# Optimization experiments

Hardware: AMD Instinct MI355X
Metric: run time of the kernel (lower is better)

The kernel has to match this reference:

```python
import jax, jax.numpy as jnp
import numpy as np

N_NODES = 100000
N_EDGES = 3200000
NUM_TYPES = 8
TYPE_DIM = 16
IN_DIM = 5
HID = 64
HEADS = 2
OUT = 64
LN_EPS = 1e-5
NEG_SLOPE = 0.2


def segment_softmax(logits, seg, num_segments):
    # logits: [E, H], seg: [E] destination ids
    m = jax.ops.segment_max(logits, seg, num_segments=num_segments)
    m = jnp.where(jnp.isfinite(m), m, 0.0)
    e = jnp.exp(logits - m[seg])
    s = jax.ops.segment_sum(e, seg, num_segments=num_segments)
    return e / (s[seg] + 1e-16)


def gat_conv(x, W, a_src, a_dst, b, src, dst, n_nodes, heads, ch):
    # x: [N, F_in], W: [F_in, heads*ch], a_src/a_dst: [heads, ch], b: [heads*ch]
    h = (x @ W).reshape(n_nodes, heads, ch)            # [N, H, C]
    al_s = jnp.einsum('nhc,hc->nh', h, a_src)          # [N, H]
    al_d = jnp.einsum('nhc,hc->nh', h, a_dst)          # [N, H]
    e = jax.nn.leaky_relu(al_s[src] + al_d[dst], NEG_SLOPE)  # [E, H]
    alpha = segment_softmax(e, dst, n_nodes)           # [E, H]
    msg = alpha[:, :, None] * h[src]                   # [E, H, C]
    out = jax.ops.segment_sum(msg, dst, num_segments=n_nodes)  # [N, H, C]
    return out.reshape(n_nodes, heads * ch) + b


def setup_inputs() -> dict:
    key = jax.random.key(0)
    ks = jax.random.split(key, 16)
    in1 = IN_DIM + TYPE_DIM  # 21
    inp = {
        'x': jax.random.normal(ks[0], (N_NODES, IN_DIM), dtype=jnp.float32),
        'edge_index': jax.random.randint(ks[1], (2, N_EDGES), 0, N_NODES, dtype=jnp.int32),
        'type_ids': jax.random.randint(ks[2], (N_NODES,), 0, NUM_TYPES, dtype=jnp.int32),
        'type_emb': jax.random.normal(ks[3], (NUM_TYPES, TYPE_DIM), dtype=jnp.float32) * 0.3,
        'W1': jax.random.normal(ks[4], (in1, HID), dtype=jnp.float32) * (1.0 / np.sqrt(in1)),
        'a_src1': jax.random.normal(ks[5], (HEADS, HID // HEADS), dtype=jnp.float32) * 0.1,
        'a_dst1': jax.random.normal(ks[6], (HEADS, HID // HEADS), dtype=jnp.float32) * 0.1,
        'b1': jnp.zeros((HID,), dtype=jnp.float32),
        'W2': jax.random.normal(ks[7], (HID, OUT), dtype=jnp.float32) * (1.0 / np.sqrt(HID)),
        'a_src2': jax.random.normal(ks[8], (1, OUT), dtype=jnp.float32) * 0.1,
        'a_dst2': jax.random.normal(ks[9], (1, OUT), dtype=jnp.float32) * 0.1,
        'b2': jnp.zeros((OUT,), dtype=jnp.float32),
        'gamma': jnp.ones((OUT,), dtype=jnp.float32),
        'beta': jnp.zeros((OUT,), dtype=jnp.float32),
    }
    return inp


def reference(x, type_emb, W1, a_src1, a_dst1, b1, W2, a_src2, a_dst2, b2, gamma, beta, edge_index, type_ids):
    n = x.shape[0]
    # type embedding concat
    xin = jnp.concatenate([x, type_emb[type_ids]], axis=1)  # [N, 21]
    # add self loops (PyG GATConv default)
    loops = jnp.arange(n, dtype=edge_index.dtype)
    src = jnp.concatenate([edge_index[0], loops])
    dst = jnp.concatenate([edge_index[1], loops])
    h = gat_conv(xin, W1, a_src1, a_dst1, b1, src, dst, n, HEADS, HID // HEADS)
    h = jax.nn.relu(h)  # dropout = identity at inference
    h = gat_conv(h, W2, a_src2, a_dst2, b2, src, dst, n, 1, OUT)
    # LayerNorm
    mu = jnp.mean(h, axis=-1, keepdims=True)
    var = jnp.var(h, axis=-1, keepdims=True)
    return (h - mu) / jnp.sqrt(var + LN_EPS) * gamma + beta
```

## Files before the change

kernel.cpp:

```cpp
#include <hip/hip_runtime.h>
#include <hip/hip_fp16.h>

#define NEG_SLOPE 0.2f
#define INVLN2 1.44269504088896f
#define BKT_SHIFT 7
#define BKT_NODES 128
#define BKT_CAP 5120
#define SRC_SHIFT 18
#define SRC_MASK 0x3FFFF
#define CHUNK 4096
#define NBMAX 1024

typedef _Float16 half8 __attribute__((ext_vector_type(8)));
typedef float float4v __attribute__((ext_vector_type(4)));

__global__ void k_bucketA(const int* __restrict__ ei, unsigned int* __restrict__ pk,
                          int* __restrict__ bcnt, int E, int NBKT)
{
    __shared__ unsigned int stage[CHUNK];
    __shared__ unsigned short stageB[CHUNK];
    __shared__ int cnt[NBMAX];
    __shared__ int excl[NBMAX];
    __shared__ int curp[NBMAX];
    __shared__ int gbase[NBMAX];

    int t = threadIdx.x;
    int e0 = blockIdx.x * CHUNK;
    bool vec4 = ((E & 3) == 0);

    for (int i = t; i < NBMAX; i += 256) cnt[i] = 0;
    __syncthreads();

    int4 s4[4], d4[4];
    bool val[4];

    if (vec4) {
#pragma unroll
        for (int it = 0; it < 4; it++) {
            int e = e0 + it * 1024 + t * 4;
            val[it] = (e < E);
            if (val[it]) {
                s4[it] = *(const int4*)(ei + e);
                d4[it] = *(const int4*)(ei + (size_t)E + e);
                atomicAdd(&cnt[d4[it].x >> BKT_SHIFT], 1);
                atomicAdd(&cnt[d4[it].y >> BKT_SHIFT], 1);
                atomicAdd(&cnt[d4[it].z >> BKT_SHIFT], 1);
                atomicAdd(&cnt[d4[it].w >> BKT_SHIFT], 1);
            }
        }
    } else {
        for (int i = t; i < CHUNK; i += 256) {
            int e = e0 + i;
            if (e >= E) break;
            atomicAdd(&cnt[ei[E + e] >> BKT_SHIFT], 1);
        }
    }
    __syncthreads();
    for (int i = t; i < NBMAX; i += 256) curp[i] = cnt[i];
    __syncthreads();
    for (int off = 1; off < NBMAX; off <<= 1) {
        int v0 = (t       >= off) ? cnt[t       - off] : 0;
        int v1 = (t + 256 >= off) ? cnt[t + 256 - off] : 0;
        int v2 = (t + 512 >= off) ? cnt[t + 512 - off] : 0;
        int v3 = (t + 768 >= off) ? cnt[t + 768 - off] : 0;
        __syncthreads();
        cnt[t] += v0; cnt[t + 256] += v1; cnt[t + 512] += v2; cnt[t + 768] += v3;
        __syncthreads();
    }
    for (int i = t; i < NBMAX; i += 256) {
        int o = curp[i];
        int ex = cnt[i] - o;
        excl[i] = ex;
        curp[i] = ex;
    }
    __syncthreads();
    for (int b = t; b < NBKT; b += 256) {
        int c = cnt[b] - excl[b];
        gbase[b] = (c > 0) ? atomicAdd(&bcnt[b], c) : 0;
    }
    __syncthreads();
    if (vec4) {
#pragma unroll
        for (int it = 0; it < 4; it++) {
            if (!val[it]) continue;
            int ss[4] = {s4[it].x, s4[it].y, s4[it].z, s4[it].w};
            int dd[4] = {d4[it].x, d4[it].y, d4[it].z, d4[it].w};
#pragma unroll
            for (int k = 0; k < 4; k++) {
                int b = dd[k] >> BKT_SHIFT;
                int p = atomicAdd(&curp[b], 1);
                stage[p] = (unsigned)ss[k] | ((unsigned)(dd[k] & (BKT_NODES - 1)) << SRC_SHIFT);
                stageB[p] = (unsigned short)b;
            }
        }
    } else {
        for (int i = t; i < CHUNK; i += 256) {
            int e = e0 + i;
            if (e >= E) break;
            int s = ei[e], d = ei[E + e];
            int b = d >> BKT_SHIFT;
            int p = atomicAdd(&curp[b], 1);
            stage[p] = (unsigned)s | ((unsigned)(d & (BKT_NODES - 1)) << SRC_SHIFT);
            stageB[p] = (unsigned short)b;
        }
    }
    __syncthreads();
    int total = E - e0; if (total > CHUNK) total = CHUNK;
    for (int i = t; i < total; i += 256) {
        int b = stageB[i];
        int idx = gbase[b] + (i - excl[b]);
        if (idx < BKT_CAP) pk[(size_t)b * BKT_CAP + idx] = stage[i];
    }
}

__global__ __launch_bounds__(256) void k_build_node1(
        const unsigned int* __restrict__ pk, const int* __restrict__ bcnt,
        int* __restrict__ rs, int* __restrict__ cur, int* __restrict__ ssrc,
        const float* __restrict__ x, const int* __restrict__ type_ids,
        const float* __restrict__ type_emb, const float* __restrict__ W1,
        const float* __restrict__ a_src1, const float* __restrict__ a_dst1,
        __half2* __restrict__ h1h, float* __restrict__ als1, float* __restrict__ ald1,
        int N, int NBKT)
{
    __shared__ unsigned int vals[BKT_CAP];
    __shared__ int cnt[BKT_NODES];
    __shared__ int cursor[BKT_NODES];
    __shared__ int orig[BKT_NODES];
    __shared__ int red[256];
    int t = threadIdx.x;

    if (blockIdx.x >= NBKT) {
        int node = (blockIdx.x - NBKT) * 4 + (t >> 6);
        int j = t & 63;
        if (node >= N) return;

        float xin[21];
#pragma unroll
        for (int k = 0; k < 5; k++) xin[k] = x[node * 5 + k];
        int ty = type_ids[node];
#pragma unroll
        for (int k = 0; k < 16; k++) xin[5 + k] = type_emb[ty * 16 + k];

        float h = 0.f;
#pragma unroll
        for (int k = 0; k < 21; k++) h += xin[k] * W1[k * 64 + j];

        float hn = __shfl_xor(h, 1);
        if ((j & 1) == 0)
            h1h[node * 32 + (j >> 1)] = __floats2half2_rn(h, hn);

        int head = j >> 5, lane = j & 31;
        float ps = h * a_src1[head * 32 + lane];
        float pd = h * a_dst1[head * 32 + lane];
#pragma unroll
        for (int m = 16; m >= 1; m >>= 1) { ps += __shfl_xor(ps, m); pd += __shfl_xor(pd, m); }
        if (lane == 0) {
            als1[node * 2 + head] = ps * INVLN2;
            ald1[node * 2 + head] = pd * INVLN2;
        }
        return;
    }

    int b = blockIdx.x;
    int nb = min(bcnt[b], BKT_CAP);

    int part = 0;
    for (int i = t; i < b; i += 256) part += min(bcnt[i], BKT_CAP);
    red[t] = part;
    if (t < BKT_NODES) cnt[t] = 0;
    __syncthreads();
    for (int off = 128; off; off >>= 1) {
        if (t < off) red[t] += red[t + off];
        __syncthreads();
    }
    int bs = red[0];

    const unsigned int* mypk = pk + (size_t)b * BKT_CAP;
    int nb4 = nb & ~3;
    for (int e = t * 4; e < nb4; e += 1024) {
        uint4 v = *(const uint4*)(mypk + e);
        *(uint4*)(vals + e) = v;
        atomicAdd(&cnt[v.x >> SRC_SHIFT], 1);
        atomicAdd(&cnt[v.y >> SRC_SHIFT], 1);
        atomicAdd(&cnt[v.z >> SRC_SHIFT], 1);
        atomicAdd(&cnt[v.w >> SRC_SHIFT], 1);
    }
    for (int e = nb4 + t; e < nb; e += 256) {
        unsigned int v = mypk[e];
        vals[e] = v;
        atomicAdd(&cnt[v >> SRC_SHIFT], 1);
    }
    __syncthreads();
    if (t < BKT_NODES) orig[t] = cnt[t];
    __syncthreads();
    for (int off = 1; off < BKT_NODES; off <<= 1) {
        int v = 0;
        if (t < BKT_NODES && t >= off) v = cnt[t - off];
        __syncthreads();
        if (t < BKT_NODES) cnt[t] += v;
        __syncthreads();
    }
    if (t < BKT_NODES) {
        int c = orig[t];
        int ex = cnt[t] - c;
        cursor[t] = ex;
        int node = (b << BKT_SHIFT) + t;
        if (node < N) { rs[node] = bs + ex; cur[node] = bs + ex + c; }
    }
    __syncthreads();
    for (int e = t; e < nb; e += 256) {
        unsigned int w = vals[e];
        int p = atomicAdd(&cursor[w >> SRC_SHIFT], 1);
        ssrc[bs + p] = (int)(w & SRC_MASK);
    }
}

__global__ void k_gather1(const int* __restrict__ rs, const int* __restrict__ cur,
                          const int* __restrict__ ssrc, const float4* __restrict__ h4,
                          const float* __restrict__ als1, const float* __restrict__ ald1,
                          const float* __restrict__ b1, float4* __restrict__ h2h4, int N)
{
    int node = blockIdx.x * 4 + (threadIdx.x >> 6);
    if (node >= N) return;
    int l = threadIdx.x & 63;
    int eg = l >> 3;
    int ch = l & 7;
    int head = ch >> 2;
    float ad = ald1[node * 2 + head];

    int beg = rs[node], end = cur[node];
    int cnt = end - beg;
    __half2 acc2[4];
    acc2[0] = acc2[1] = acc2[2] = acc2[3] = __float2half2_rn(0.f);
    float wsum = 0.f;

    int s0c = (eg < cnt) ? ssrc[beg + eg] : node;
    int s1c = (8 + eg < cnt) ? ssrc[beg + 8 + eg] : node;
    float al0c = als1[s0c * 2 + head];
    float al1c = als1[s1c * 2 + head];
    float4 r0c = h4[(size_t)s0c * 8 + ch];
    float4 r1c = h4[(size_t)s1c * 8 + ch];

    for (int base = 0; base < cnt; base += 16) {
        int n0 = base + 16 + eg, n1 = base + 24 + eg;
        int s0n = (n0 < cnt) ? ssrc[beg + n0] : node;
        int s1n = (n1 < cnt) ? ssrc[beg + n1] : node;
        float al0n = als1[s0n * 2 + head];
        float al1n = als1[s1n * 2 + head];
        float4 r0n = h4[(size_t)s0n * 8 + ch];
        float4 r1n = h4[(size_t)s1n * 8 + ch];

        bool v0 = (base + eg) < cnt, v1 = (base + 8 + eg) < cnt;
        float lg0 = al0c + ad; lg0 = (lg0 >= 0.f) ? lg0 : NEG_SLOPE * lg0;
        float lg1 = al1c + ad; lg1 = (lg1 >= 0.f) ? lg1 : NEG_SLOPE * lg1;
        float w0 = v0 ? exp2f(lg0) : 0.f;
        float w1 = v1 ? exp2f(lg1) : 0.f;
        __half2 wh0 = __float2half2_rn(w0);
        __half2 wh1 = __float2half2_rn(w1);
        const __half2* p0 = (const __half2*)&r0c;
        const __half2* p1 = (const __half2*)&r1c;
#pragma unroll
        for (int q = 0; q < 4; q++) {
            acc2[q] = __hfma2(p0[q], wh0, acc2[q]);
            acc2[q] = __hfma2(p1[q], wh1, acc2[q]);
        }
        wsum += w0 + w1;

        s0c = s0n; s1c = s1n; al0c = al0n; al1c = al1n; r0c = r0n; r1c = r1n;
    }
    float acc[8];
#pragma unroll
    for (int q = 0; q < 4; q++) {
        float2 f = __half22float2(acc2[q]);
        acc[2*q] = f.x; acc[2*q+1] = f.y;
    }
#pragma unroll
    for (int m = 8; m <= 32; m <<= 1) {
        wsum += __shfl_xor(wsum, m);
#pragma unroll
        for (int q = 0; q < 8; q++) acc[q] += __shfl_xor(acc[q], m);
    }
    {
        float lg = als1[node * 2 + head] + ad;
        lg = (lg >= 0.f) ? lg : NEG_SLOPE * lg;
        float w = exp2f(lg);
        float4 r = h4[(size_t)node * 8 + ch];
        const __half2* p = (const __half2*)&r;
#pragma unroll
        for (int q = 0; q < 4; q++) {
            float2 f = __half22float2(p[q]);
            acc[2*q] += w * f.x; acc[2*q+1] += w * f.y;
        }
        wsum += w;
    }
    float inv = 1.f / (wsum + 1e-16f);
    if (eg == 0) {
        union { float4 f4; __half2 h2[4]; } u;
#pragma unroll
        for (int q = 0; q < 4; q++) {
            float v0 = fmaxf(acc[2*q]   * inv + b1[ch * 8 + 2*q],     0.f);
            float v1 = fmaxf(acc[2*q+1] * inv + b1[ch * 8 + 2*q + 1], 0.f);
            u.h2[q] = __floats2half2_rn(v0, v1);
        }
        h2h4[(size_t)node * 8 + ch] = u.f4;
    }
}

__global__ __launch_bounds__(256) void k_node2m(
        const _Float16* __restrict__ h2h, const float* __restrict__ W2,
        const float* __restrict__ a_src2, const float* __restrict__ a_dst2,
        _Float16* __restrict__ h3h, float* __restrict__ als2, float* __restrict__ ald2, int N)
{
    __shared__ _Float16 w2t[64][72];
    __shared__ float h3t[4][16][65];
    int t = threadIdx.x;
    for (int e = t; e < 4096; e += 256) {
        int k = e >> 6, n = e & 63;
        w2t[n][k] = (_Float16)W2[e];
    }
    __syncthreads();

    int w = t >> 6, l = t & 63;
    int l15 = l & 15, quad = l >> 4;
    int nodebase = blockIdx.x * 64 + w * 16;

    int arow = nodebase + l15;
    if (arow >= N) arow = N - 1;
    const half8* ap = (const half8*)(h2h + (size_t)arow * 64 + quad * 8);
    half8 a0 = ap[0];
    half8 a1 = ap[4];
    float4v accs[4];
#pragma unroll
    for (int nt = 0; nt < 4; nt++) {
        half8 b0 = *(const half8*)(&w2t[nt * 16 + l15][quad * 8]);
        half8 b1 = *(const half8*)(&w2t[nt * 16 + l15][32 + quad * 8]);
        float4v c = {0.f, 0.f, 0.f, 0.f};
        c = __builtin_amdgcn_mfma_f32_16x16x32_f16(a0, b0, c, 0, 0, 0);
        c = __builtin_amdgcn_mfma_f32_16x16x32_f16(a1, b1, c, 0, 0, 0);
        accs[nt] = c;
    }
#pragma unroll
    for (int nt = 0; nt < 4; nt++)
#pragma unroll
        for (int r = 0; r < 4; r++)
            h3t[w][quad * 4 + r][nt * 16 + l15] = accs[nt][r];
    __syncthreads();

    int m = l >> 2, part = l & 3;
    int g = blockIdx.x * 64 + w * 16 + m;
    float ps = 0.f, pd = 0.f;
    union { float4 f4[2]; _Float16 h[16]; } u;
#pragma unroll
    for (int c = 0; c < 16; c++) {
        float v = h3t[w][m][part * 16 + c];
        ps += v * a_src2[part * 16 + c];
        pd += v * a_dst2[part * 16 + c];
        u.h[c] = (_Float16)v;
    }
    if (g < N) {
        float4* dst = (float4*)(h3h + (size_t)g * 64) + part * 2;
        dst[0] = u.f4[0];
        dst[1] = u.f4[1];
    }
    ps += __shfl_xor(ps, 1); ps += __shfl_xor(ps, 2);
    pd += __shfl_xor(pd, 1); pd += __shfl_xor(pd, 2);
    if (part == 0 && g < N) { als2[g] = ps * INVLN2; ald2[g] = pd * INVLN2; }
}

__global__ void k_gather2(const int* __restrict__ rs, const int* __restrict__ cur,
                          const int* __restrict__ ssrc, const float4* __restrict__ h4,
                          const float* __restrict__ als2, const float* __restrict__ ald2,
                          const float* __restrict__ b2, const float* __restrict__ gamma,
                          const float* __restrict__ beta, float* __restrict__ out, int N)
{
    int node = blockIdx.x * 4 + (threadIdx.x >> 6);
    if (node >= N) return;
    int l = threadIdx.x & 63;
    int eg = l >> 3;
    int ch = l & 7;
    float ad = ald2[node];

    int beg = rs[node], end = cur[node];
    int cnt = end - beg;
    __half2 acc2[4];
    acc2[0] = acc2[1] = acc2[2] = acc2[3] = __float2half2_rn(0.f);
    float wsum = 0.f;

    int s0c = (eg < cnt) ? ssrc[beg + eg] : node;
    int s1c = (8 + eg < cnt) ? ssrc[beg + 8 + eg] : node;
    float al0c = als2[s0c];
    float al1c = als2[s1c];
    float4 r0c = h4[(size_t)s0c * 8 + ch];
    float4 r1c = h4[(size_t)s1c * 8 + ch];

    for (int base = 0; base < cnt; base += 16) {
        int n0 = base + 16 + eg, n1 = base + 24 + eg;
        int s0n = (n0 < cnt) ? ssrc[beg + n0] : node;
        int s1n = (n1 < cnt) ? ssrc[beg + n1] : node;
        float al0n = als2[s0n];
        float al1n = als2[s1n];
        float4 r0n = h4[(size_t)s0n * 8 + ch];
        float4 r1n = h4[(size_t)s1n * 8 + ch];

        bool v0 = (base + eg) < cnt, v1 = (base + 8 + eg) < cnt;
        float lg0 = al0c + ad; lg0 = (lg0 >= 0.f) ? lg0 : NEG_SLOPE * lg0;
        float lg1 = al1c + ad; lg1 = (lg1 >= 0.f) ? lg1 : NEG_SLOPE * lg1;
        float w0 = v0 ? exp2f(lg0) : 0.f;
        float w1 = v1 ? exp2f(lg1) : 0.f;
        __half2 wh0 = __float2half2_rn(w0);
        __half2 wh1 = __float2half2_rn(w1);
        const __half2* p0 = (const __half2*)&r0c;
        const __half2* p1 = (const __half2*)&r1c;
#pragma unroll
        for (int q = 0; q < 4; q++) {
            acc2[q] = __hfma2(p0[q], wh0, acc2[q]);
            acc2[q] = __hfma2(p1[q], wh1, acc2[q]);
        }
        wsum += w0 + w1;

        s0c = s0n; s1c = s1n; al0c = al0n; al1c = al1n; r0c = r0n; r1c = r1n;
    }
    float acc[8];
#pragma unroll
    for (int q = 0; q < 4; q++) {
        float2 f = __half22float2(acc2[q]);
        acc[2*q] = f.x; acc[2*q+1] = f.y;
    }
#pragma unroll
    for (int m = 8; m <= 32; m <<= 1) {
        wsum += __shfl_xor(wsum, m);
#pragma unroll
        for (int q = 0; q < 8; q++) acc[q] += __shfl_xor(acc[q], m);
    }
    {
        float lg = als2[node] + ad;
        lg = (lg >= 0.f) ? lg : NEG_SLOPE * lg;
        float w = exp2f(lg);
        float4 r = h4[(size_t)node * 8 + ch];
        const __half2* p = (const __half2*)&r;
#pragma unroll
        for (int q = 0; q < 4; q++) {
            float2 f = __half22float2(p[q]);
            acc[2*q] += w * f.x; acc[2*q+1] += w * f.y;
        }
        wsum += w;
    }
    float inv = 1.f / (wsum + 1e-16f);
    float o[8];
    float s = 0.f;
#pragma unroll
    for (int q = 0; q < 8; q++) { o[q] = acc[q] * inv + b2[ch * 8 + q]; s += o[q]; }
#pragma unroll
    for (int m = 1; m <= 4; m <<= 1) s += __shfl_xor(s, m);
    float mu = s * (1.f / 64.f);
    float v = 0.f;
#pragma unroll
    for (int q = 0; q < 8; q++) { float d = o[q] - mu; v += d * d; }
#pragma unroll
    for (int m = 1; m <= 4; m <<= 1) v += __shfl_xor(v, m);
    v *= (1.f / 64.f);
    float r = rsqrtf(v + 1e-5f);
    if (eg == 0) {
        float res[8];
#pragma unroll
        for (int q = 0; q < 8; q++)
            res[q] = (o[q] - mu) * r * gamma[ch * 8 + q] + beta[ch * 8 + q];
        float4* op = (float4*)(out + (size_t)node * 64 + ch * 8);
        op[0] = make_float4(res[0], res[1], res[2], res[3]);
        op[1] = make_float4(res[4], res[5], res[6], res[7]);
    }
}

extern "C" void kernel_launch(void* const* d_in, const int* in_sizes, int n_in,
                              void* d_out, int out_size, void* d_ws, size_t ws_size,
                              hipStream_t stream) {
    const float* x        = (const float*)d_in[0];
    const int*   ei       = (const int*)  d_in[1];
    const int*   type_ids = (const int*)  d_in[2];
    const float* type_emb = (const float*)d_in[3];
    const float* W1       = (const float*)d_in[4];
    const float* a_src1   = (const float*)d_in[5];
    const float* a_dst1   = (const float*)d_in[6];
    const float* b1       = (const float*)d_in[7];
    const float* W2       = (const float*)d_in[8];
    const float* a_src2   = (const float*)d_in[9];
    const float* a_dst2   = (const float*)d_in[10];
    const float* b2       = (const float*)d_in[11];
    const float* gamma    = (const float*)d_in[12];
    const float* beta     = (const float*)d_in[13];

    int N = in_sizes[0] / 5;
    int E = in_sizes[1] / 2;
    int NBKT = (N + BKT_NODES - 1) >> BKT_SHIFT;

    char* base = (char*)d_ws;
    size_t off = 0;
    auto carve = [&](size_t bytes) { void* p = base + off; off += (bytes + 255) & ~(size_t)255; return p; };
    __half2* h1h = (__half2*)carve((size_t)N * 64 * sizeof(__half));
    size_t pk_bytes = (size_t)NBKT * BKT_CAP * sizeof(unsigned int);
    size_t h23_bytes = 2 * (size_t)N * 64 * sizeof(__half);
    char* uni = (char*)carve(pk_bytes > h23_bytes ? pk_bytes : h23_bytes);
    _Float16* h2h = (_Float16*)uni;
    _Float16* h3h = (_Float16*)(uni + (size_t)N * 64 * sizeof(__half));
    unsigned int* pk = (unsigned int*)uni;
    float* als1  = (float*)carve((size_t)N * 2 * sizeof(float));
    float* ald1  = (float*)carve((size_t)N * 2 * sizeof(float));
    float* als2  = (float*)carve((size_t)N * sizeof(float));
    float* ald2  = (float*)carve((size_t)N * sizeof(float));
    int*   rs    = (int*)carve((size_t)N * sizeof(int));
    int*   cur   = (int*)carve((size_t)N * sizeof(int));
    int*   bcnt  = (int*)carve(1024 * sizeof(int));
    int*   ssrc  = (int*)carve((size_t)E * sizeof(int));

    dim3 tb(256);
    dim3 nb((N + 3) / 4);
    int nodeBlocks = (N + 3) / 4;

    hipMemsetAsync(bcnt, 0, NBKT * sizeof(int), stream);
    k_bucketA<<<dim3((E + CHUNK - 1) / CHUNK), tb, 0, stream>>>(ei, pk, bcnt, E, NBKT);

    k_build_node1<<<dim3(NBKT + nodeBlocks), tb, 0, stream>>>(
        pk, bcnt, rs, cur, ssrc,
        x, type_ids, type_emb, W1, a_src1, a_dst1, h1h, als1, ald1,
        N, NBKT);

    k_gather1<<<nb, tb, 0, stream>>>(rs, cur, ssrc, (const float4*)h1h, als1, ald1, b1,
                                     (float4*)h2h, N);
    k_node2m<<<dim3((N + 63) / 64), tb, 0, stream>>>(h2h, W2, a_src2, a_dst2,
                                                     h3h, als2, ald2, N);
    k_gather2<<<nb, tb, 0, stream>>>(rs, cur, ssrc, (const float4*)h3h, als2, ald2, b2,
                                     gamma, beta, (float*)d_out, N);
}
```

Measured before the change: 316.8 us.

## Compute edge weights once per edge and share via LDS in gather kernels

Each wavefront now loads up to 64 source indices and attention logits per batch, one edge per lane, computes both heads' softmax weights once, and stages indices and weights in shared memory. The 8-lane groups then read them back to gather feature rows. Before, every lane recomputed the logits and exp for its edge and loaded the logits redundantly. The change drops the software-pipelined prefetch of the next rows, which can expose gather latency. It also relies on LDS writes and reads inside one wavefront without explicit barriers.

```diff
diff --git a/kernel.cpp b/kernel.cpp
--- a/kernel.cpp
+++ b/kernel.cpp
@@ -220,53 +220,57 @@
                           const float* __restrict__ als1, const float* __restrict__ ald1,
                           const float* __restrict__ b1, float4* __restrict__ h2h4, int N)
 {
-    int node = blockIdx.x * 4 + (threadIdx.x >> 6);
+    __shared__ int    sS[4][64];
+    __shared__ float2 sW[4][64];
+    int wv = threadIdx.x >> 6;
+    int node = blockIdx.x * 4 + wv;
     if (node >= N) return;
     int l = threadIdx.x & 63;
     int eg = l >> 3;
     int ch = l & 7;
     int head = ch >> 2;
-    float ad = ald1[node * 2 + head];
+    float2 ad = ((const float2*)ald1)[node];
 
     int beg = rs[node], end = cur[node];
     int cnt = end - beg;
+    const int* sp = ssrc + beg;
     __half2 acc2[4];
     acc2[0] = acc2[1] = acc2[2] = acc2[3] = __float2half2_rn(0.f);
-    float wsum = 0.f;
-
-    int s0c = (eg < cnt) ? ssrc[beg + eg] : node;
-    int s1c = (8 + eg < cnt) ? ssrc[beg + 8 + eg] : node;
-    float al0c = als1[s0c * 2 + head];
-    float al1c = als1[s1c * 2 + head];
-    float4 r0c = h4[(size_t)s0c * 8 + ch];
-    float4 r1c = h4[(size_t)s1c * 8 + ch];
-
-    for (int base = 0; base < cnt; base += 16) {
-        int n0 = base + 16 + eg, n1 = base + 24 + eg;
-        int s0n = (n0 < cnt) ? ssrc[beg + n0] : node;
-        int s1n = (n1 < cnt) ? ssrc[beg + n1] : node;
-        float al0n = als1[s0n * 2 + head];
-        float al1n = als1[s1n * 2 + head];
-        float4 r0n = h4[(size_t)s0n * 8 + ch];
-        float4 r1n = h4[(size_t)s1n * 8 + ch];
-
-        bool v0 = (base + eg) < cnt, v1 = (base + 8 + eg) < cnt;
-        float lg0 = al0c + ad; lg0 = (lg0 >= 0.f) ? lg0 : NEG_SLOPE * lg0;
-        float lg1 = al1c + ad; lg1 = (lg1 >= 0.f) ? lg1 : NEG_SLOPE * lg1;
-        float w0 = v0 ? exp2f(lg0) : 0.f;
-        float w1 = v1 ? exp2f(lg1) : 0.f;
-        __half2 wh0 = __float2half2_rn(w0);
-        __half2 wh1 = __float2half2_rn(w1);
-        const __half2* p0 = (const __half2*)&r0c;
-        const __half2* p1 = (const __half2*)&r1c;
-#pragma unroll
-        for (int q = 0; q < 4; q++) {
-            acc2[q] = __hfma2(p0[q], wh0, acc2[q]);
-            acc2[q] = __hfma2(p1[q], wh1, acc2[q]);
-        }
-        wsum += w0 + w1;
-
-        s0c = s0n; s1c = s1n; al0c = al0n; al1c = al1n; r0c = r0n; r1c = r1n;
+    float ws0 = 0.f, ws1 = 0.f;
+
+    for (int base = 0; base < cnt; base += 64) {
+        int e = base + l;
+        bool v = e < cnt;
+        int s = v ? sp[e] : node;
+        float2 al = ((const float2*)als1)[s];
+        float lg0 = al.x + ad.x; lg0 = (lg0 >= 0.f) ? lg0 : NEG_SLOPE * lg0;
+        float lg1 = al.y + ad.y; lg1 = (lg1 >= 0.f) ? lg1 : NEG_SLOPE * lg1;
+        float w0 = v ? exp2f(lg0) : 0.f;
+        float w1 = v ? exp2f(lg1) : 0.f;
+        sS[wv][l] = s;
+        sW[wv][l] = make_float2(w0, w1);
+        ws0 += w0; ws1 += w1;
+
+        int rem = cnt - base;
+        const float* sWf = (const float*)&sW[wv][0];
+        for (int sub = 0; sub < 8 && sub * 8 < rem; sub += 2) {
+            int i0 = sub * 8 + eg, i1 = i0 + 8;
+            int sA = sS[wv][i0];
+            int sB = sS[wv][i1];
+            float wA = sWf[i0 * 2 + head];
+            float wB = sWf[i1 * 2 + head];
+            float4 rA = h4[(size_t)sA * 8 + ch];
+            float4 rB = h4[(size_t)sB * 8 + ch];
+            __half2 whA = __float2half2_rn(wA);
+            __half2 whB = __float2half2_rn(wB);
+            const __half2* pA = (const __half2*)&rA;
+            const __half2* pB = (const __half2*)&rB;
+#pragma unroll
+            for (int q = 0; q < 4; q++) {
+                acc2[q] = __hfma2(pA[q], whA, acc2[q]);
+                acc2[q] = __hfma2(pB[q], whB, acc2[q]);
+            }
+        }
     }
     float acc[8];
 #pragma unroll
@@ -275,13 +279,16 @@
         acc[2*q] = f.x; acc[2*q+1] = f.y;
     }
 #pragma unroll
+    for (int m = 1; m <= 32; m <<= 1) { ws0 += __shfl_xor(ws0, m); ws1 += __shfl_xor(ws1, m); }
+#pragma unroll
     for (int m = 8; m <= 32; m <<= 1) {
-        wsum += __shfl_xor(wsum, m);
 #pragma unroll
         for (int q = 0; q < 8; q++) acc[q] += __shfl_xor(acc[q], m);
     }
+    float wsum = head ? ws1 : ws0;
     {
-        float lg = als1[node * 2 + head] + ad;
+        float2 al = ((const float2*)als1)[node];
+        float lg = (head ? al.y + ad.y : al.x + ad.x);
         lg = (lg >= 0.f) ? lg : NEG_SLOPE * lg;
         float w = exp2f(lg);
         float4 r = h4[(size_t)node * 8 + ch];
@@ -373,7 +380,10 @@
                           const float* __restrict__ b2, const float* __restrict__ gamma,
                           const float* __restrict__ beta, float* __restrict__ out, int N)
 {
-    int node = blockIdx.x * 4 + (threadIdx.x >> 6);
+    __shared__ int   sS[4][64];
+    __shared__ float sW[4][64];
+    int wv = threadIdx.x >> 6;
+    int node = blockIdx.x * 4 + wv;
     if (node >= N) return;
     int l = threadIdx.x & 63;
     int eg = l >> 3;
@@ -382,43 +392,40 @@
 
     int beg = rs[node], end = cur[node];
     int cnt = end - beg;
+    const int* sp = ssrc + beg;
     __half2 acc2[4];
     acc2[0] = acc2[1] = acc2[2] = acc2[3] = __float2half2_rn(0.f);
-    float wsum = 0.f;
-
-    int s0c = (eg < cnt) ? ssrc[beg + eg] : node;
-    int s1c = (8 + eg < cnt) ? ssrc[beg + 8 + eg] : node;
-    float al0c = als2[s0c];
-    float al1c = als2[s1c];
-    float4 r0c = h4[(size_t)s0c * 8 + ch];
-    float4 r1c = h4[(size_t)s1c * 8 + ch];
-
-    for (int base = 0; base < cnt; base += 16) {
-        int n0 = base + 16 + eg, n1 = base + 24 + eg;
-        int s0n = (n0 < cnt) ? ssrc[beg + n0] : node;
-        int s1n = (n1 < cnt) ? ssrc[beg + n1] : node;
-        float al0n = als2[s0n];
-        float al1n = als2[s1n];
-        float4 r0n = h4[(size_t)s0n * 8 + ch];
-        float4 r1n = h4[(size_t)s1n * 8 + ch];
-
-        bool v0 = (base + eg) < cnt, v1 = (base + 8 + eg) < cnt;
-        float lg0 = al0c + ad; lg0 = (lg0 >= 0.f) ? lg0 : NEG_SLOPE * lg0;
-        float lg1 = al1c + ad; lg1 = (lg1 >= 0.f) ? lg1 : NEG_SLOPE * lg1;
-        float w0 = v0 ? exp2f(lg0) : 0.f;
-        float w1 = v1 ? exp2f(lg1) : 0.f;
-        __half2 wh0 = __float2half2_rn(w0);
-        __half2 wh1 = __float2half2_rn(w1);
-        const __half2* p0 = (const __half2*)&r0c;
-        const __half2* p1 = (const __half2*)&r1c;
-#pragma unroll
-        for (int q = 0; q < 4; q++) {
-            acc2[q] = __hfma2(p0[q], wh0, acc2[q]);
-            acc2[q] = __hfma2(p1[q], wh1, acc2[q]);
-        }
-        wsum += w0 + w1;
-
-        s0c = s0n; s1c = s1n; al0c = al0n; al1c = al1n; r0c = r0n; r1c = r1n;
+    float ws = 0.f;
+
+    for (int base = 0; base < cnt; base += 64) {
+        int e = base + l;
+        bool v = e < cnt;
+        int s = v ? sp[e] : node;
+        float lg = als2[s] + ad; lg = (lg >= 0.f) ? lg : NEG_SLOPE * lg;
+        float w = v ? exp2f(lg) : 0.f;
+        sS[wv][l] = s;
+        sW[wv][l] = w;
+        ws += w;
+
+        int rem = cnt - base;
+        for (int sub = 0; sub < 8 && sub * 8 < rem; sub += 2) {
+            int i0 = sub * 8 + eg, i1 = i0 + 8;
+            int sA = sS[wv][i0];
+            int sB = sS[wv][i1];
+            float wA = sW[wv][i0];
+            float wB = sW[wv][i1];
+            float4 rA = h4[(size_t)sA * 8 + ch];
+            float4 rB = h4[(size_t)sB * 8 + ch];
+            __half2 whA = __float2half2_rn(wA);
+            __half2 whB = __float2half2_rn(wB);
+            const __half2* pA = (const __half2*)&rA;
+            const __half2* pB = (const __half2*)&rB;
+#pragma unroll
+            for (int q = 0; q < 4; q++) {
+                acc2[q] = __hfma2(pA[q], whA, acc2[q]);
+                acc2[q] = __hfma2(pB[q], whB, acc2[q]);
+            }
+        }
     }
     float acc[8];
 #pragma unroll
@@ -427,8 +434,9 @@
         acc[2*q] = f.x; acc[2*q+1] = f.y;
     }
 #pragma unroll
+    for (int m = 1; m <= 32; m <<= 1) ws += __shfl_xor(ws, m);
+#pragma unroll
     for (int m = 8; m <= 32; m <<= 1) {
-        wsum += __shfl_xor(wsum, m);
 #pragma unroll
         for (int q = 0; q < 8; q++) acc[q] += __shfl_xor(acc[q], m);
     }
@@ -443,9 +451,9 @@
             float2 f = __half22float2(p[q]);
             acc[2*q] += w * f.x; acc[2*q+1] += w * f.y;
         }
-        wsum += w;
-    }
-    float inv = 1.f / (wsum + 1e-16f);
+        ws += w;
+    }
+    float inv = 1.f / (ws + 1e-16f);
     float o[8];
     float s = 0.f;
 #pragma unroll
```

After: 326.6 us. 3.1% more time.
